# Optimization experiments

Hardware: AMD Instinct MI355X
Metric: run time of the kernel (lower is better)

## Reference

```python
import jax, jax.numpy as jnp
import numpy as np

N_NODES = 100000
LEAKY_SLOPE = 0.01  # nn.LeakyReLU default

def setup_inputs() -> dict:
    key = jax.random.key(0)
    k1, k2, k3, k4, k5, k6 = jax.random.split(key, 6)
    in_dim, out_dim, ef_dim = 64, 64, 32
    E = 500000
    nf = jax.random.normal(k1, (N_NODES, in_dim), dtype=jnp.float32)
    ef = jax.random.normal(k2, (E, ef_dim), dtype=jnp.float32)
    src = jax.random.randint(k3, (E,), 0, N_NODES, dtype=jnp.int64 if jax.config.jax_enable_x64 else jnp.int32)
    dst = jax.random.randint(k4, (E,), 0, N_NODES, dtype=src.dtype)
    # torch Linear weights: (out, in), no bias
    We = jax.random.normal(k5, (out_dim, 2 * in_dim + ef_dim), dtype=jnp.float32) * 0.05
    Wn = jax.random.normal(k6, (out_dim, out_dim + in_dim), dtype=jnp.float32) * 0.05
    return {"nf": nf, "ef": ef, "src": src, "dst": dst, "We": We, "Wn": Wn}

def reference(nf, ef, src, dst, We, Wn):
    # Module adds reverse edges sharing the same edge features
    src_all = jnp.concatenate([src, dst])          # [2E]
    dst_all = jnp.concatenate([dst, src])          # [2E]
    ef_all = jnp.concatenate([ef, ef], axis=0)     # [2E, ef_dim]
    # message: concat(src_nf, dst_nf, ef) -> Linear -> LeakyReLU
    m_in = jnp.concatenate([nf[src_all], nf[dst_all], ef_all], axis=-1)  # [2E, 2*in+ef]
    msg = jax.nn.leaky_relu(m_in @ We.T, negative_slope=LEAKY_SLOPE)     # [2E, out]
    # reduce: sum messages at destination nodes
    red = jax.ops.segment_sum(msg, dst_all, num_segments=N_NODES)       # [N, out]
    # apply: concat(nf, red_msg) -> Linear -> LeakyReLU
    n_in = jnp.concatenate([nf, red], axis=-1)                          # [N, in+out]
    out_nf = jax.nn.leaky_relu(n_in @ Wn.T, negative_slope=LEAKY_SLOPE)
    return out_nf
```

## Files before the change

kernel.cpp:

```cpp
#include <hip/hip_runtime.h>
#include <stdint.h>


#define LEAKY(x) fmaxf((x), 0.01f * (x))
#define CAP 40
typedef _Float16 f16;
typedef _Float16 h2 __attribute__((ext_vector_type(2)));
typedef int iv4 __attribute__((ext_vector_type(4)));

static __device__ __forceinline__ int swz(int k, int c) {
    return k * 128 + (c ^ (((k >> 2) & 7) << 2));
}

union H4 { f16 h[4]; h2 p[2]; short4 s; long long ll; };

__global__ void prep_weights_kernel(const float* __restrict__ We,
                                    const float* __restrict__ Wn,
                                    float* __restrict__ WTab,
                                    float* __restrict__ WTc,
                                    float* __restrict__ WTn,
                                    int* __restrict__ cnt, int N)
{
    const int stride = gridDim.x * blockDim.x;
    int i = blockIdx.x * blockDim.x + threadIdx.x;
    for (int j = i; j < 8192 + 2048 + 8192; j += stride) {
        if (j < 8192) {
            int k = j >> 7, n = j & 127;
            WTab[j] = We[(n & 63) * 160 + (n >> 6) * 64 + k];
        } else if (j < 10240) {
            int q = j - 8192; int k = q >> 6, n = q & 63;
            WTc[q] = We[n * 160 + 128 + k];
        } else {
            int q = j - 10240; int k = q >> 6, n = q & 63;
            WTn[q] = Wn[n * 128 + k];
        }
    }
    const int C4 = N * 4;
    for (int j = i; j < C4; j += stride) cnt[j] = 0;
}

__global__ __launch_bounds__(256) void gemm_ab_kernel(
    const float4* __restrict__ nf4, const float* __restrict__ WT,
    f16* __restrict__ A16, f16* __restrict__ B16, int M)
{
    __shared__ float As[64 * 128];
    __shared__ float Ws[64 * 128];
    const int t = threadIdx.x;
    const int tr = t >> 4, tc = t & 15;
    const int m0 = blockIdx.x * 128;

    #pragma unroll
    for (int i = 0; i < 8; ++i)
        ((float4*)Ws)[t + 256 * i] = ((const float4*)WT)[t + 256 * i];
    #pragma unroll
    for (int i = 0; i < 8; ++i) {
        const int idx = t + 256 * i;
        const int m = idx >> 4, kq = idx & 15;
        float4 v = make_float4(0.f, 0.f, 0.f, 0.f);
        if (m0 + m < M) v = nf4[(size_t)(m0 + m) * 16 + kq];
        As[swz(4 * kq + 0, m)] = v.x;
        As[swz(4 * kq + 1, m)] = v.y;
        As[swz(4 * kq + 2, m)] = v.z;
        As[swz(4 * kq + 3, m)] = v.w;
    }
    __syncthreads();

    float acc[8][8];
    #pragma unroll
    for (int ri = 0; ri < 8; ++ri)
        #pragma unroll
        for (int ci = 0; ci < 8; ++ci) acc[ri][ci] = 0.f;

    #pragma unroll 8
    for (int k = 0; k < 64; ++k) {
        const float4 aLo = *(const float4*)&As[swz(k, tr * 4)];
        const float4 aHi = *(const float4*)&As[swz(k, 64 + tr * 4)];
        const float4 bLo = *(const float4*)&Ws[k * 128 + tc * 4];
        const float4 bHi = *(const float4*)&Ws[k * 128 + 64 + tc * 4];
        const float av[8] = {aLo.x, aLo.y, aLo.z, aLo.w, aHi.x, aHi.y, aHi.z, aHi.w};
        const float bv[8] = {bLo.x, bLo.y, bLo.z, bLo.w, bHi.x, bHi.y, bHi.z, bHi.w};
        #pragma unroll
        for (int ri = 0; ri < 8; ++ri)
            #pragma unroll
            for (int ci = 0; ci < 8; ++ci) acc[ri][ci] += av[ri] * bv[ci];
    }

    #pragma unroll
    for (int ri = 0; ri < 8; ++ri) {
        const int v = m0 + ((ri < 4) ? (tr * 4 + ri) : (64 + tr * 4 + ri - 4));
        if (v < M) {
            H4 lo, hi;
            #pragma unroll
            for (int j = 0; j < 4; ++j) { lo.h[j] = (f16)acc[ri][j]; hi.h[j] = (f16)acc[ri][4 + j]; }
            *(short4*)&A16[(size_t)v * 64 + tc * 4] = lo.s;
            *(short4*)&B16[(size_t)v * 64 + tc * 4] = hi.s;
        }
    }
}

__global__ __launch_bounds__(256) void gemm_p_kernel(
    const float4* __restrict__ nf4, const float* __restrict__ WTn,
    f16* __restrict__ P16, int M)
{
    __shared__ float As[64 * 128];
    __shared__ float Ws[64 * 64];
    const int t = threadIdx.x;
    const int tr = t >> 4, tc = t & 15;
    const int m0 = blockIdx.x * 128;

    #pragma unroll
    for (int i = 0; i < 4; ++i)
        ((float4*)Ws)[t + 256 * i] = ((const float4*)WTn)[t + 256 * i];
    #pragma unroll
    for (int i = 0; i < 8; ++i) {
        const int idx = t + 256 * i;
        const int m = idx >> 4, kq = idx & 15;
        float4 v = make_float4(0.f, 0.f, 0.f, 0.f);
        if (m0 + m < M) v = nf4[(size_t)(m0 + m) * 16 + kq];
        As[swz(4 * kq + 0, m)] = v.x;
        As[swz(4 * kq + 1, m)] = v.y;
        As[swz(4 * kq + 2, m)] = v.z;
        As[swz(4 * kq + 3, m)] = v.w;
    }
    __syncthreads();

    float acc[8][4];
    #pragma unroll
    for (int ri = 0; ri < 8; ++ri)
        #pragma unroll
        for (int ci = 0; ci < 4; ++ci) acc[ri][ci] = 0.f;

    #pragma unroll 8
    for (int k = 0; k < 64; ++k) {
        const float4 aLo = *(const float4*)&As[swz(k, tr * 4)];
        const float4 aHi = *(const float4*)&As[swz(k, 64 + tr * 4)];
        const float4 w  = *(const float4*)&Ws[k * 64 + tc * 4];
        const float av[8] = {aLo.x, aLo.y, aLo.z, aLo.w, aHi.x, aHi.y, aHi.z, aHi.w};
        const float bv[4] = {w.x, w.y, w.z, w.w};
        #pragma unroll
        for (int ri = 0; ri < 8; ++ri)
            #pragma unroll
            for (int ci = 0; ci < 4; ++ci) acc[ri][ci] += av[ri] * bv[ci];
    }

    #pragma unroll
    for (int ri = 0; ri < 8; ++ri) {
        const int v = m0 + ((ri < 4) ? (tr * 4 + ri) : (64 + tr * 4 + ri - 4));
        if (v < M) {
            H4 u;
            #pragma unroll
            for (int j = 0; j < 4; ++j) u.h[j] = (f16)acc[ri][j];
            *(short4*)&P16[(size_t)v * 64 + tc * 4] = u.s;
        }
    }
}

__global__ __launch_bounds__(256) void gemm_c_kernel(
    const float4* __restrict__ ef4, const float* __restrict__ WT,
    f16* __restrict__ C16, int M)
{
    __shared__ float As[32 * 128];
    __shared__ float Ws[32 * 64];
    const int t = threadIdx.x;
    const int tr = t >> 4, tc = t & 15;
    const int m0 = blockIdx.x * 128;

    #pragma unroll
    for (int i = 0; i < 2; ++i)
        ((float4*)Ws)[t + 256 * i] = ((const float4*)WT)[t + 256 * i];
    #pragma unroll
    for (int i = 0; i < 4; ++i) {
        const int idx = t + 256 * i;
        const int m = idx >> 3, kq = idx & 7;
        float4 v = make_float4(0.f, 0.f, 0.f, 0.f);
        if (m0 + m < M) v = ef4[(size_t)(m0 + m) * 8 + kq];
        As[swz(4 * kq + 0, m)] = v.x;
        As[swz(4 * kq + 1, m)] = v.y;
        As[swz(4 * kq + 2, m)] = v.z;
        As[swz(4 * kq + 3, m)] = v.w;
    }
    __syncthreads();

    float acc[8][4];
    #pragma unroll
    for (int ri = 0; ri < 8; ++ri)
        #pragma unroll
        for (int ci = 0; ci < 4; ++ci) acc[ri][ci] = 0.f;

    #pragma unroll 8
    for (int k = 0; k < 32; ++k) {
        const float4 aLo = *(const float4*)&As[swz(k, tr * 4)];
        const float4 aHi = *(const float4*)&As[swz(k, 64 + tr * 4)];
        const float4 w  = *(const float4*)&Ws[k * 64 + tc * 4];
        const float av[8] = {aLo.x, aLo.y, aLo.z, aLo.w, aHi.x, aHi.y, aHi.z, aHi.w};
        const float bv[4] = {w.x, w.y, w.z, w.w};
        #pragma unroll
        for (int ri = 0; ri < 8; ++ri)
            #pragma unroll
            for (int ci = 0; ci < 4; ++ci) acc[ri][ci] += av[ri] * bv[ci];
    }

    #pragma unroll
    for (int ri = 0; ri < 8; ++ri) {
        const int v = m0 + ((ri < 4) ? (tr * 4 + ri) : (64 + tr * 4 + ri - 4));
        if (v < M) {
            H4 u;
            #pragma unroll
            for (int j = 0; j < 4; ++j) u.h[j] = (f16)acc[ri][j];
            *(short4*)&C16[(size_t)v * 64 + tc * 4] = u.s;
        }
    }
}

__global__ __launch_bounds__(256) void scatter_kernel(
    const int* __restrict__ src, const int* __restrict__ dst,
    int* __restrict__ cnt, int2* __restrict__ inc, int E, int N)
{
    const int part = blockIdx.x & 7;
    const int lo = (int)(((long long)N * part) >> 3);
    const int hi = (int)(((long long)N * (part + 1)) >> 3);
    const int tid = (blockIdx.x >> 3) * blockDim.x + threadIdx.x;
    const int tpp = (gridDim.x >> 3) * blockDim.x;
    const int E4 = E >> 2;
    const iv4* src4 = (const iv4*)src;
    const iv4* dst4 = (const iv4*)dst;
    #define PUT(node, nbr, eid) \
        if ((node) >= lo && (node) < hi) { \
            const int p = atomicAdd(&cnt[(node) * 4], 1); \
            if (p < CAP) inc[(size_t)(node) * CAP + p] = make_int2((nbr) << 7, (eid) << 7); \
        }
    for (int j = tid; j < E4; j += tpp) {
        const iv4 s = __builtin_nontemporal_load(&src4[j]);
        const iv4 d = __builtin_nontemporal_load(&dst4[j]);
        const int e0 = 4 * j;
        PUT(d.x, s.x, e0 + 0)
        PUT(d.y, s.y, e0 + 1)
        PUT(d.z, s.z, e0 + 2)
        PUT(d.w, s.w, e0 + 3)
        PUT(s.x, d.x, e0 + 0)
        PUT(s.y, d.y, e0 + 1)
        PUT(s.z, d.z, e0 + 2)
        PUT(s.w, d.w, e0 + 3)
    }
    for (int i = (E4 << 2) + tid; i < E; i += tpp) {
        const int s = src[i], d = dst[i];
        PUT(d, s, i)
        PUT(s, d, i)
    }
    #undef PUT
}

__global__ __launch_bounds__(256) void reduce_kernel(
    const f16* __restrict__ A16, const f16* __restrict__ B16,
    const f16* __restrict__ C16, const int* __restrict__ cnt,
    const int2* __restrict__ inc, f16* __restrict__ red16, int N)
{
    const int lane = threadIdx.x & 63;
    const int g = lane >> 4;
    const int sub = lane & 15;
    const int sub8 = sub * 8;
    const char* Ab = (const char*)A16;
    const char* Cb = (const char*)C16;
    const int gw = (blockIdx.x * blockDim.x + threadIdx.x) >> 6;
    const int W = (gridDim.x * blockDim.x) >> 6;
    const int NQ = (N + 3) >> 2;
    const _Float16 k01 = (_Float16)0.01f;
    const h2 c001 = {k01, k01};
    for (int q = gw; q < NQ; q += W) {
        const int v = q * 4 + g;
        const int vc = (v < N) ? v : (N - 1);
        const int len = min(cnt[vc * 4], CAP);
        const int ebase = vc * CAP;
        H4 bh; bh.s = *(const short4*)&B16[(size_t)vc * 64 + sub * 4];
        const h2 b0 = bh.p[0], b1 = bh.p[1];
        int mx = (len + 7) >> 3;
        mx = max(mx, __shfl_xor(mx, 16));
        mx = max(mx, __shfl_xor(mx, 32));
        float a0 = 0.f, a1 = 0.f, a2 = 0.f, a3 = 0.f;
        for (int it = 0; it < mx; ++it) {
            const int el = it * 8;
            const int4 q0 = *(const int4*)&inc[ebase + el];
            const int4 q1 = *(const int4*)&inc[ebase + el + 2];
            const int4 q2 = *(const int4*)&inc[ebase + el + 4];
            const int4 q3 = *(const int4*)&inc[ebase + el + 6];
            float okf[8];
            unsigned ao[8], co[8];
            #pragma unroll
            for (int k2 = 0; k2 < 8; ++k2)
                okf[k2] = ((unsigned)(el + k2) < (unsigned)len) ? 1.0f : 0.0f;
            const int qa[8] = {q0.x, q0.z, q1.x, q1.z, q2.x, q2.z, q3.x, q3.z};
            const int qc[8] = {q0.y, q0.w, q1.y, q1.w, q2.y, q2.w, q3.y, q3.w};
            #pragma unroll
            for (int k2 = 0; k2 < 8; ++k2) {
                ao[k2] = (okf[k2] != 0.0f) ? (unsigned)qa[k2] : 0u;
                co[k2] = (okf[k2] != 0.0f) ? (unsigned)qc[k2] : 0u;
            }
            H4 Av[8], Cv[8];
            #pragma unroll
            for (int k2 = 0; k2 < 8; ++k2) {
                Av[k2].s = *(const short4*)(Ab + (size_t)ao[k2] + sub8);
                Cv[k2].s = *(const short4*)(Cb + (size_t)co[k2] + sub8);
            }
            #pragma unroll
            for (int k2 = 0; k2 < 8; ++k2) {
                h2 s0 = Av[k2].p[0] + Cv[k2].p[0] + b0;
                h2 s1 = Av[k2].p[1] + Cv[k2].p[1] + b1;
                s0 = __builtin_elementwise_max(s0, s0 * c001);
                s1 = __builtin_elementwise_max(s1, s1 * c001);
                a0 = fmaf((float)s0[0], okf[k2], a0);
                a1 = fmaf((float)s0[1], okf[k2], a1);
                a2 = fmaf((float)s1[0], okf[k2], a2);
                a3 = fmaf((float)s1[1], okf[k2], a3);
            }
        }
        if (v < N) {
            H4 u;
            u.h[0] = (f16)a0; u.h[1] = (f16)a1; u.h[2] = (f16)a2; u.h[3] = (f16)a3;
            *(short4*)&red16[(size_t)v * 64 + sub * 4] = u.s;
        }
    }
}

__global__ __launch_bounds__(256) void apply_lite_kernel(
    const f16* __restrict__ red16, const f16* __restrict__ P16,
    const float* __restrict__ WTn, float* __restrict__ out, int M)
{
    __shared__ float As[64 * 128];
    __shared__ float Ws[64 * 64];
    const int t = threadIdx.x;
    const int tr = t >> 4, tc = t & 15;
    const int m0 = blockIdx.x * 128;
    const float* WT1 = WTn + 4096;

    #pragma unroll
    for (int i = 0; i < 4; ++i)
        ((float4*)Ws)[t + 256 * i] = ((const float4*)WT1)[t + 256 * i];
    #pragma unroll
    for (int i = 0; i < 8; ++i) {
        const int idx = t + 256 * i;
        const int m = idx >> 4, kq = idx & 15;
        H4 v; v.ll = 0;
        if (m0 + m < M) v.s = *(const short4*)&red16[(size_t)(m0 + m) * 64 + kq * 4];
        As[swz(4 * kq + 0, m)] = (float)v.h[0];
        As[swz(4 * kq + 1, m)] = (float)v.h[1];
        As[swz(4 * kq + 2, m)] = (float)v.h[2];
        As[swz(4 * kq + 3, m)] = (float)v.h[3];
    }
    __syncthreads();

    float acc[8][4];
    #pragma unroll
    for (int ri = 0; ri < 8; ++ri)
        #pragma unroll
        for (int ci = 0; ci < 4; ++ci) acc[ri][ci] = 0.f;

    #pragma unroll 8
    for (int k = 0; k < 64; ++k) {
        const float4 aLo = *(const float4*)&As[swz(k, tr * 4)];
        const float4 aHi = *(const float4*)&As[swz(k, 64 + tr * 4)];
        const float4 w  = *(const float4*)&Ws[k * 64 + tc * 4];
        const float av[8] = {aLo.x, aLo.y, aLo.z, aLo.w, aHi.x, aHi.y, aHi.z, aHi.w};
        const float bv[4] = {w.x, w.y, w.z, w.w};
        #pragma unroll
        for (int ri = 0; ri < 8; ++ri)
            #pragma unroll
            for (int ci = 0; ci < 4; ++ci) acc[ri][ci] += av[ri] * bv[ci];
    }

    #pragma unroll
    for (int ri = 0; ri < 8; ++ri) {
        const int v = m0 + ((ri < 4) ? (tr * 4 + ri) : (64 + tr * 4 + ri - 4));
        if (v < M) {
            H4 pv; pv.s = *(const short4*)&P16[(size_t)v * 64 + tc * 4];
            float4 o;
            o.x = LEAKY(acc[ri][0] + (float)pv.h[0]);
            o.y = LEAKY(acc[ri][1] + (float)pv.h[1]);
            o.z = LEAKY(acc[ri][2] + (float)pv.h[2]);
            o.w = LEAKY(acc[ri][3] + (float)pv.h[3]);
            *(float4*)&out[(size_t)v * 64 + tc * 4] = o;
        }
    }
}

extern "C" void kernel_launch(void* const* d_in, const int* in_sizes, int n_in,
                              void* d_out, int out_size, void* d_ws, size_t ws_size,
                              hipStream_t stream) {
    const float* nf  = (const float*)d_in[0];
    const float* ef  = (const float*)d_in[1];
    const int*   src = (const int*)d_in[2];
    const int*   dst = (const int*)d_in[3];
    const float* We  = (const float*)d_in[4];
    const float* Wn  = (const float*)d_in[5];

    const int N = in_sizes[0] / 64;
    const int E = in_sizes[2];

    char* p = (char*)d_ws;
    auto alloc = [&](size_t bytes) -> char* {
        char* r = p; p += (bytes + 255) & ~(size_t)255; return r;
    };
    f16*   red16 = (f16*)alloc((size_t)N * 64 * 2);
    float* WTab  = (float*)alloc(8192 * 4);
    float* WTc   = (float*)alloc(2048 * 4);
    float* WTn   = (float*)alloc(8192 * 4);
    int2*  inc   = (int2*)alloc((size_t)N * CAP * 8);
    int*   cnt   = (int*)alloc((size_t)N * 4 * 4);
    f16*   A16   = (f16*)alloc((size_t)N * 64 * 2);
    f16*   B16   = (f16*)alloc((size_t)N * 64 * 2);
    f16*   C16   = (f16*)alloc((size_t)E * 64 * 2);
    f16*   P16   = (f16*)alloc((size_t)N * 64 * 2);

    const int NQ = (N + 3) >> 2;

    prep_weights_kernel<<<512, 256, 0, stream>>>(We, Wn, WTab, WTc, WTn, cnt, N);
    gemm_c_kernel<<<(E + 127) / 128, 256, 0, stream>>>((const float4*)ef, WTc, C16, E);
    gemm_ab_kernel<<<(N + 127) / 128, 256, 0, stream>>>((const float4*)nf, WTab, A16, B16, N);
    gemm_p_kernel<<<(N + 127) / 128, 256, 0, stream>>>((const float4*)nf, WTn, P16, N);
    scatter_kernel<<<2048, 256, 0, stream>>>(src, dst, cnt, inc, E, N);
    reduce_kernel<<<(NQ + 3) / 4, 256, 0, stream>>>(A16, B16, C16, cnt, inc, red16, N);
    apply_lite_kernel<<<(N + 127) / 128, 256, 0, stream>>>(red16, P16, WTn, (float*)d_out, N);
}
```

Measured before the change: 322.0 us.

## Widen reduce gathers to 16B, partition nodes by XCD, zero-init incidence list

The reduce kernel now gives each node 8 lanes that load 16 bytes per gathered row, in place of 16 lanes loading 8 bytes, and steps through 4 edges per iteration instead of 8. Blocks are split into 8 interleaved partitions so each block-index residue handles a contiguous range of nodes, which appears aimed at L2 locality across the chiplets. The incidence buffer is now zeroed in the prep kernel, and the scatter kernel runs before the GEMMs. Zeroing adds extra write traffic, and the smaller edge step lowers memory-level parallelism per lane.

```diff
diff --git a/kernel.cpp b/kernel.cpp
--- a/kernel.cpp
+++ b/kernel.cpp
@@ -13,13 +13,15 @@
 }
 
 union H4 { f16 h[4]; h2 p[2]; short4 s; long long ll; };
+union H8 { f16 h[8]; h2 p[4]; int4 q; };
 
 __global__ void prep_weights_kernel(const float* __restrict__ We,
                                     const float* __restrict__ Wn,
                                     float* __restrict__ WTab,
                                     float* __restrict__ WTc,
                                     float* __restrict__ WTn,
-                                    int* __restrict__ cnt, int N)
+                                    int* __restrict__ cnt,
+                                    int4* __restrict__ inc4, int N)
 {
     const int stride = gridDim.x * blockDim.x;
     int i = blockIdx.x * blockDim.x + threadIdx.x;
@@ -37,6 +39,9 @@
     }
     const int C4 = N * 4;
     for (int j = i; j < C4; j += stride) cnt[j] = 0;
+    const int I4 = N * (CAP / 2);
+    const int4 z = make_int4(0, 0, 0, 0);
+    for (int j = i; j < I4; j += stride) inc4[j] = z;
 }
 
 __global__ __launch_bounds__(256) void gemm_ab_kernel(
@@ -256,67 +261,79 @@
     const int2* __restrict__ inc, f16* __restrict__ red16, int N)
 {
     const int lane = threadIdx.x & 63;
-    const int g = lane >> 4;
-    const int sub = lane & 15;
-    const int sub8 = sub * 8;
+    const int g = lane >> 3;
+    const int sub = lane & 7;
+    const int sub16 = sub * 16;
     const char* Ab = (const char*)A16;
     const char* Cb = (const char*)C16;
-    const int gw = (blockIdx.x * blockDim.x + threadIdx.x) >> 6;
-    const int W = (gridDim.x * blockDim.x) >> 6;
-    const int NQ = (N + 3) >> 2;
+    const int part = blockIdx.x & 7;
+    const int NO = (N + 7) >> 3;
+    const int olo = (int)(((long long)NO * part) >> 3);
+    const int ohi = (int)(((long long)NO * (part + 1)) >> 3);
+    const int wid = (((blockIdx.x >> 3) * blockDim.x) + threadIdx.x) >> 6;
+    const int wstride = ((gridDim.x >> 3) * blockDim.x) >> 6;
     const _Float16 k01 = (_Float16)0.01f;
     const h2 c001 = {k01, k01};
-    for (int q = gw; q < NQ; q += W) {
-        const int v = q * 4 + g;
+    for (int oct = olo + wid; oct < ohi; oct += wstride) {
+        const int v = oct * 8 + g;
         const int vc = (v < N) ? v : (N - 1);
         const int len = min(cnt[vc * 4], CAP);
         const int ebase = vc * CAP;
-        H4 bh; bh.s = *(const short4*)&B16[(size_t)vc * 64 + sub * 4];
-        const h2 b0 = bh.p[0], b1 = bh.p[1];
-        int mx = (len + 7) >> 3;
+        H8 bh; bh.q = *(const int4*)&B16[(size_t)vc * 64 + sub * 8];
+        const h2 b0 = bh.p[0], b1 = bh.p[1], b2 = bh.p[2], b3 = bh.p[3];
+        int mx = (len + 3) >> 2;
+        mx = max(mx, __shfl_xor(mx, 8));
         mx = max(mx, __shfl_xor(mx, 16));
         mx = max(mx, __shfl_xor(mx, 32));
         float a0 = 0.f, a1 = 0.f, a2 = 0.f, a3 = 0.f;
+        float a4 = 0.f, a5 = 0.f, a6 = 0.f, a7 = 0.f;
         for (int it = 0; it < mx; ++it) {
-            const int el = it * 8;
+            const int el = it * 4;
             const int4 q0 = *(const int4*)&inc[ebase + el];
             const int4 q1 = *(const int4*)&inc[ebase + el + 2];
-            const int4 q2 = *(const int4*)&inc[ebase + el + 4];
-            const int4 q3 = *(const int4*)&inc[ebase + el + 6];
-            float okf[8];
-            unsigned ao[8], co[8];
-            #pragma unroll
-            for (int k2 = 0; k2 < 8; ++k2)
+            float okf[4];
+            unsigned ao[4], co[4];
+            #pragma unroll
+            for (int k2 = 0; k2 < 4; ++k2)
                 okf[k2] = ((unsigned)(el + k2) < (unsigned)len) ? 1.0f : 0.0f;
-            const int qa[8] = {q0.x, q0.z, q1.x, q1.z, q2.x, q2.z, q3.x, q3.z};
-            const int qc[8] = {q0.y, q0.w, q1.y, q1.w, q2.y, q2.w, q3.y, q3.w};
-            #pragma unroll
-            for (int k2 = 0; k2 < 8; ++k2) {
+            const int qa[4] = {q0.x, q0.z, q1.x, q1.z};
+            const int qc[4] = {q0.y, q0.w, q1.y, q1.w};
+            #pragma unroll
+            for (int k2 = 0; k2 < 4; ++k2) {
                 ao[k2] = (okf[k2] != 0.0f) ? (unsigned)qa[k2] : 0u;
                 co[k2] = (okf[k2] != 0.0f) ? (unsigned)qc[k2] : 0u;
             }
-            H4 Av[8], Cv[8];
-            #pragma unroll
-            for (int k2 = 0; k2 < 8; ++k2) {
-                Av[k2].s = *(const short4*)(Ab + (size_t)ao[k2] + sub8);
-                Cv[k2].s = *(const short4*)(Cb + (size_t)co[k2] + sub8);
+            H8 Av[4], Cv[4];
+            #pragma unroll
+            for (int k2 = 0; k2 < 4; ++k2) {
+                Av[k2].q = *(const int4*)(Ab + (size_t)ao[k2] + sub16);
+                Cv[k2].q = *(const int4*)(Cb + (size_t)co[k2] + sub16);
             }
             #pragma unroll
-            for (int k2 = 0; k2 < 8; ++k2) {
+            for (int k2 = 0; k2 < 4; ++k2) {
                 h2 s0 = Av[k2].p[0] + Cv[k2].p[0] + b0;
                 h2 s1 = Av[k2].p[1] + Cv[k2].p[1] + b1;
+                h2 s2 = Av[k2].p[2] + Cv[k2].p[2] + b2;
+                h2 s3 = Av[k2].p[3] + Cv[k2].p[3] + b3;
                 s0 = __builtin_elementwise_max(s0, s0 * c001);
                 s1 = __builtin_elementwise_max(s1, s1 * c001);
+                s2 = __builtin_elementwise_max(s2, s2 * c001);
+                s3 = __builtin_elementwise_max(s3, s3 * c001);
                 a0 = fmaf((float)s0[0], okf[k2], a0);
                 a1 = fmaf((float)s0[1], okf[k2], a1);
                 a2 = fmaf((float)s1[0], okf[k2], a2);
                 a3 = fmaf((float)s1[1], okf[k2], a3);
+                a4 = fmaf((float)s2[0], okf[k2], a4);
+                a5 = fmaf((float)s2[1], okf[k2], a5);
+                a6 = fmaf((float)s3[0], okf[k2], a6);
+                a7 = fmaf((float)s3[1], okf[k2], a7);
             }
         }
         if (v < N) {
-            H4 u;
+            H8 u;
             u.h[0] = (f16)a0; u.h[1] = (f16)a1; u.h[2] = (f16)a2; u.h[3] = (f16)a3;
-            *(short4*)&red16[(size_t)v * 64 + sub * 4] = u.s;
+            u.h[4] = (f16)a4; u.h[5] = (f16)a5; u.h[6] = (f16)a6; u.h[7] = (f16)a7;
+            *(int4*)&red16[(size_t)v * 64 + sub * 8] = u.q;
         }
     }
 }
@@ -410,13 +427,15 @@
     f16*   C16   = (f16*)alloc((size_t)E * 64 * 2);
     f16*   P16   = (f16*)alloc((size_t)N * 64 * 2);
 
-    const int NQ = (N + 3) >> 2;
-
-    prep_weights_kernel<<<512, 256, 0, stream>>>(We, Wn, WTab, WTc, WTn, cnt, N);
+    const int NO = (N + 7) >> 3;
+    const int redBlocks = (((NO + 3) / 4) + 7) & ~7;
+
+    prep_weights_kernel<<<1024, 256, 0, stream>>>(We, Wn, WTab, WTc, WTn, cnt,
+                                                  (int4*)inc, N);
+    scatter_kernel<<<2048, 256, 0, stream>>>(src, dst, cnt, inc, E, N);
     gemm_c_kernel<<<(E + 127) / 128, 256, 0, stream>>>((const float4*)ef, WTc, C16, E);
     gemm_ab_kernel<<<(N + 127) / 128, 256, 0, stream>>>((const float4*)nf, WTab, A16, B16, N);
     gemm_p_kernel<<<(N + 127) / 128, 256, 0, stream>>>((const float4*)nf, WTn, P16, N);
-    scatter_kernel<<<2048, 256, 0, stream>>>(src, dst, cnt, inc, E, N);
-    reduce_kernel<<<(NQ + 3) / 4, 256, 0, stream>>>(A16, B16, C16, cnt, inc, red16, N);
+    reduce_kernel<<<redBlocks, 256, 0, stream>>>(A16, B16, C16, cnt, inc, red16, N);
     apply_lite_kernel<<<(N + 127) / 128, 256, 0, stream>>>(red16, P16, WTn, (float*)d_out, N);
 }
```

After: 314.9 us. 1.02x faster.
